# Kernel optimization log

Measured on AMD Instinct MI355X. Metric: run time of the kernel, lower is better.

The kernel has to match this reference:

```python
import math
import jax, jax.numpy as jnp
import numpy as np

T_LEN, BSZ, E_DIM, N_HEADS = 2048, 4, 768, 12


def setup_inputs() -> dict:
    key = jax.random.key(0)
    k0, k1, k2 = jax.random.split(key, 3)
    E = E_DIM
    return {
        "query": jax.random.normal(k0, (T_LEN, BSZ, E), dtype=jnp.float32),
        "attn_mask": jnp.zeros((T_LEN, T_LEN), dtype=jnp.float32),
        "in_proj_weight": jax.random.normal(k1, (3 * E, E), dtype=jnp.float32) * (1.0 / math.sqrt(E)),
        "in_proj_bias": jnp.zeros((3 * E,), dtype=jnp.float32),
        "out_proj_weight": jax.random.normal(k2, (E, E), dtype=jnp.float32) * (1.0 / math.sqrt(E)),
        "out_proj_bias": jnp.zeros((E,), dtype=jnp.float32),
        "num_heads": N_HEADS,
    }


def _rope_tables(seq_len, head_dim, dtype):
    # position_enc[pos, j] = pos / 10000**(2j/head_dim), j in [0, head_dim//2)
    pos = jnp.arange(seq_len, dtype=jnp.float32)[:, None]
    j = jnp.arange(head_dim // 2, dtype=jnp.float32)[None, :]
    ang = pos / jnp.power(jnp.float32(10000.0), 2.0 * j / head_dim)
    # stack([x, x], -1).reshape == repeat-interleave by 2 along last dim
    sin = jnp.repeat(jnp.sin(ang), 2, axis=-1).astype(dtype)  # (S, hd)
    cos = jnp.repeat(jnp.cos(ang), 2, axis=-1).astype(dtype)
    return sin, cos


def _rotate_half(x):
    # interleaved pairs: (x0, x1, x2, x3, ...) -> (-x1, x0, -x3, x2, ...)
    x_even = x[..., 0::2]
    x_odd = x[..., 1::2]
    return jnp.stack([-x_odd, x_even], axis=-1).reshape(x.shape)


def reference(query, attn_mask, in_proj_weight, in_proj_bias, out_proj_weight, out_proj_bias, num_heads):
    T, B, E = query.shape
    H = num_heads
    hd = E // H

    # fused QKV in-projection: (T, B, 3E)
    proj = jnp.einsum('tbe,fe->tbf', query, in_proj_weight) + in_proj_bias
    q, k, v = jnp.split(proj, 3, axis=-1)  # each (T, B, E)

    def to_bhtd(x):
        return jnp.transpose(x.reshape(T, B, H, hd), (1, 2, 0, 3))  # (B, H, T, hd)

    q, k, v = to_bhtd(q), to_bhtd(k), to_bhtd(v)

    sin, cos = _rope_tables(T, hd, q.dtype)  # (T, hd), broadcast over (B, H)
    q = q * cos + _rotate_half(q) * sin
    k = k * cos + _rotate_half(k) * sin

    scale = 1.0 / math.sqrt(hd)
    scores = jnp.einsum('bhtd,bhsd->bhts', q, k) * scale + attn_mask[None, None, :, :]
    attn = jax.nn.softmax(scores, axis=-1)
    out = jnp.einsum('bhts,bhsd->bhtd', attn, v)  # (B, H, T, hd)

    out = jnp.transpose(out, (2, 0, 1, 3)).reshape(T * B, E)  # (T*B, E)
    out = out @ out_proj_weight.T + out_proj_bias
    return out.reshape(T, B, E)
```

## Files before the change

kernel.cpp:

```cpp
#include <hip/hip_runtime.h>
#include <math.h>

#define TLEN 2048
#define BSZ  4
#define EDIM 768
#define NH   12
#define HD   64
#define NBH  (BSZ * NH)
#define LOG2E 1.44269504088896f

typedef __bf16 bf16;
typedef __bf16 bf16x8 __attribute__((ext_vector_type(8)));
typedef float  f32x4  __attribute__((ext_vector_type(4)));
typedef unsigned int uint;

__device__ __forceinline__ f32x4 mfma16(bf16x8 a, bf16x8 b, f32x4 c) {
  return __builtin_amdgcn_mfma_f32_16x16x32_bf16(a, b, c, 0, 0, 0);
}

__device__ __forceinline__ uint cvtpk(float lo, float hi) {
  uint r;
  asm("v_cvt_pk_bf16_f32 %0, %1, %2" : "=v"(r) : "v"(lo), "v"(hi));
  return r;
}

#define GLD16(gp, lp)                                                          \
  __builtin_amdgcn_global_load_lds(                                            \
      (const __attribute__((address_space(1))) uint32_t*)(gp),                 \
      (__attribute__((address_space(3))) uint32_t*)(lp), 16, 0, 0)

__device__ __forceinline__ bf16x8 ldsfrag(const bf16* t, int row, int kb) {
  return *reinterpret_cast<const bf16x8*>(
      (const char*)t + row * 128 + (kb ^ ((row & 7) << 4)));
}

#define CT_OFF   0x0u
#define ST_OFF   0x40000u
#define FLG_OFF  0x80000u
#define AQ_OFF   0x100000u
#define XB_OFF   0x100000u
#define QB_OFF   0xD00000u
#define KB_OFF   0x1900000u
#define VT_OFF   0x2500000u
#define WI_OFF   0x3100000u
#define WO_OFF   0x3460000u

#define QN8  786432
#define WIN8 221184
#define WON8 73728

__device__ __forceinline__ void cvt8(const float* __restrict__ s,
                                     bf16* __restrict__ d, int i) {
  const float4* sp = reinterpret_cast<const float4*>(s) + (size_t)i * 2;
  float4 a = sp[0], b = sp[1];
  bf16x8 o;
  o[0] = (bf16)a.x; o[1] = (bf16)a.y; o[2] = (bf16)a.z; o[3] = (bf16)a.w;
  o[4] = (bf16)b.x; o[5] = (bf16)b.y; o[6] = (bf16)b.z; o[7] = (bf16)b.w;
  reinterpret_cast<bf16x8*>(d)[i] = o;
}

__global__ __launch_bounds__(256) void prep_all_kernel(
    const float* __restrict__ q, bf16* __restrict__ qo,
    const float* __restrict__ wi, bf16* __restrict__ wio,
    const float* __restrict__ wo, bf16* __restrict__ woo,
    const float* __restrict__ mask, uint* __restrict__ flags,
    float* __restrict__ ct, float* __restrict__ st) {
  int bid = blockIdx.x;
  int tid = threadIdx.x;
  if (bid < 256) {
    int i = bid * 256 + tid;
    int t = i >> 5, j = i & 31;
    double ang = (double)t * pow(10000.0, -(double)j / 32.0);
    st[i] = (float)sin(ang);
    ct[i] = (float)cos(ang);
  } else if (bid < 4480) {
    int i = (bid - 256) * 256 + tid;
    if (i < QN8) { cvt8(q, qo, i); return; }
    int j = i - QN8;
    if (j < WIN8) { cvt8(wi, wio, j); return; }
    cvt8(wo, woo, j - WIN8);
  } else {
    int tile = bid - 4480;
    int ty = tile >> 5, tx = tile & 31;
    uint acc = 0;
#pragma unroll
    for (int i = 0; i < 4; ++i) {
      int c = tid + 256 * i;
      int rr = c >> 4, cc = (c & 15) * 4;
      float4 v = *reinterpret_cast<const float4*>(
          mask + (size_t)(ty * 64 + rr) * TLEN + tx * 64 + cc);
      acc |= __float_as_uint(v.x) | __float_as_uint(v.y) |
             __float_as_uint(v.z) | __float_as_uint(v.w);
    }
    unsigned long long b = __ballot(acc != 0);
    __shared__ uint red[4];
    if ((tid & 63) == 0) red[tid >> 6] = (b != 0ull) ? 1u : 0u;
    __syncthreads();
    if (tid == 0) flags[tile] = red[0] | red[1] | red[2] | red[3];
  }
}

template <int MODE>
__global__ __launch_bounds__(256) void gemm_bt(
    const bf16* __restrict__ A, const bf16* __restrict__ B,
    const float* __restrict__ bias,
    const float* __restrict__ ct, const float* __restrict__ st,
    bf16* __restrict__ qo, bf16* __restrict__ ko, bf16* __restrict__ vo,
    float* __restrict__ fo) {
  constexpr int K = EDIM;
  __shared__ __align__(16) bf16 As[128 * 64];
  __shared__ __align__(16) bf16 Bs[128 * 64];
  int tid = threadIdx.x;
  int lane = tid & 63, w = tid >> 6;
  int wr = w >> 1, wc = w & 1;
  int g = lane >> 4, cl = lane & 15;
  int bm = blockIdx.y, bn = blockIdx.x;
  int lrow = lane >> 3;
  int colb = ((lane & 7) ^ lrow) << 4;
  const char* Abase = (const char*)(A + (size_t)bm * 128 * K);
  const char* Bbase = (const char*)(B + (size_t)bn * 128 * K);

  f32x4 acc[4][4] = {};

  for (int kt = 0; kt < K; kt += 64) {
#pragma unroll
    for (int i = 0; i < 4; ++i) {
      int qi = w * 4 + i;
      int row = qi * 8 + lrow;
      GLD16(Abase + (size_t)row * (K * 2) + kt * 2 + colb, As + qi * 512 + lane * 8);
      GLD16(Bbase + (size_t)row * (K * 2) + kt * 2 + colb, Bs + qi * 512 + lane * 8);
    }
    __syncthreads();
#pragma unroll
    for (int kk = 0; kk < 2; ++kk) {
      bf16x8 af[4], bfr[4];
#pragma unroll
      for (int mi = 0; mi < 4; ++mi)
        af[mi] = ldsfrag(As, wr * 64 + mi * 16 + cl, kk * 64 + g * 16);
#pragma unroll
      for (int ni = 0; ni < 4; ++ni)
        bfr[ni] = ldsfrag(Bs, wc * 64 + ni * 16 + cl, kk * 64 + g * 16);
#pragma unroll
      for (int mi = 0; mi < 4; ++mi)
#pragma unroll
        for (int ni = 0; ni < 4; ++ni)
          acc[mi][ni] = mfma16(af[mi], bfr[ni], acc[mi][ni]);
    }
    __syncthreads();
  }

  if (MODE == 0) {
#pragma unroll
    for (int mi = 0; mi < 4; ++mi) {
      int mbase = bm * 128 + wr * 64 + mi * 16 + 4 * g;
      int t = mbase >> 2;
      int tl = t & 63;
      int tp = (t & ~63) + 32 * ((tl >> 5) & 1) + 8 * ((tl >> 2) & 3) +
               4 * ((tl >> 4) & 1) + (tl & 3);
#pragma unroll
      for (int ni = 0; ni < 4; ++ni) {
        int f = bn * 128 + wc * 64 + ni * 16 + cl;
        int sec = f / EDIM;
        int f0 = f - sec * EDIM;
        int h = f0 >> 6, d = f0 & 63;
        float bv = bias[f];
        float vals[4];
#pragma unroll
        for (int r = 0; r < 4; ++r) vals[r] = acc[mi][ni][r] + bv;
        if (sec < 2) {
          int j = d >> 1;
          float cv = ct[t * 32 + j], sv = st[t * 32 + j];
          bf16* dst = (sec == 0) ? qo : ko;
#pragma unroll
          for (int r = 0; r < 4; ++r) {
            float other = __shfl_xor(vals[r], 1);
            float rv = (d & 1) ? (vals[r] * cv + other * sv)
                               : (vals[r] * cv - other * sv);
            if (sec == 0) rv *= 0.125f * LOG2E;
            dst[(((size_t)r * NH + h) * TLEN + t) * HD + d] = (bf16)rv;
          }
        } else {
#pragma unroll
          for (int r = 0; r < 4; ++r)
            vo[(((size_t)r * NH + h) * HD + d) * TLEN + tp] = (bf16)vals[r];
        }
      }
    }
  } else {
#pragma unroll
    for (int mi = 0; mi < 4; ++mi) {
      int mbase = bm * 128 + wr * 64 + mi * 16 + 4 * g;
#pragma unroll
      for (int ni = 0; ni < 4; ++ni) {
        int n = bn * 128 + wc * 64 + ni * 16 + cl;
        float bv = bias[n];
#pragma unroll
        for (int r = 0; r < 4; ++r)
          fo[(size_t)(mbase + r) * EDIM + n] = acc[mi][ni][r] + bv;
      }
    }
  }
}

__global__ __launch_bounds__(512) void attn_kernel(
    const bf16* __restrict__ qa, const bf16* __restrict__ ka,
    const bf16* __restrict__ vt, const float* __restrict__ mask,
    const uint* __restrict__ flags, bf16* __restrict__ xo) {
  __shared__ __align__(16) bf16 Ks[2][4096];
  __shared__ __align__(16) bf16 Vs[2][4096];
  int tid = threadIdx.x;
  int lane = tid & 63, w = tid >> 6;
  int g = lane >> 4, cl = lane & 15;
  int lin = blockIdx.y * 16 + blockIdx.x;
  int lin2 = (lin & 7) * 96 + (lin >> 3);
  int qt = lin2 & 15, bh = lin2 >> 4;
  int qrow0 = qt * 128 + w * 16;
  const bf16* qbh = qa + (size_t)bh * TLEN * HD;
  const char* kbase = (const char*)(ka + (size_t)bh * TLEN * HD);
  const char* vbase = (const char*)(vt + (size_t)bh * HD * TLEN);
  int lrow = lane >> 3;
  int colb = ((lane & 7) ^ lrow) << 4;
  int sw = w & 3;
  const uint* flgrow = flags + (qrow0 >> 6) * 32;

  bf16x8 qf[2];
#pragma unroll
  for (int h = 0; h < 2; ++h)
    qf[h] = *reinterpret_cast<const bf16x8*>(
        qbh + (size_t)(qrow0 + cl) * HD + h * 32 + g * 8);

  bf16x8 ones;
#pragma unroll
  for (int j = 0; j < 8; ++j) ones[j] = (bf16)1.0f;

  f32x4 o[4] = {};
  f32x4 oden = {};
  float mrow = -1e30f;

#pragma unroll
  for (int i = 0; i < 2; ++i) {
    int qi = sw * 2 + i;
    int row = qi * 8 + lrow;
    if (w < 4)
      GLD16(kbase + (size_t)row * 128 + colb, &Ks[0][qi * 512 + lane * 8]);
    else
      GLD16(vbase + (size_t)row * (TLEN * 2) + colb, &Vs[0][qi * 512 + lane * 8]);
  }
  __syncthreads();

  for (int stile = 0; stile < TLEN / 64; ++stile) {
    int cur = stile & 1;
    if (stile + 1 < TLEN / 64) {
      int s1 = (stile + 1) * 64;
#pragma unroll
      for (int i = 0; i < 2; ++i) {
        int qi = sw * 2 + i;
        int row = qi * 8 + lrow;
        if (w < 4)
          GLD16(kbase + (size_t)(s1 + row) * 128 + colb,
                &Ks[cur ^ 1][qi * 512 + lane * 8]);
        else
          GLD16(vbase + (size_t)row * (TLEN * 2) + s1 * 2 + colb,
                &Vs[cur ^ 1][qi * 512 + lane * 8]);
      }
    }
    const bf16* Kc = Ks[cur];
    const bf16* Vc = Vs[cur];

    f32x4 sc[4];
#pragma unroll
    for (int ni = 0; ni < 4; ++ni) {
      bf16x8 k0 = ldsfrag(Kc, ni * 16 + cl, g * 16);
      bf16x8 k1 = ldsfrag(Kc, ni * 16 + cl, 64 + g * 16);
      f32x4 z = {};
      z = mfma16(k0, qf[0], z);
      z = mfma16(k1, qf[1], z);
      sc[ni] = z;
    }

    if (flgrow[stile]) {
      int q = qrow0 + cl;
#pragma unroll
      for (int ni = 0; ni < 4; ++ni)
#pragma unroll
        for (int r = 0; r < 4; ++r)
          sc[ni][r] = fmaf(mask[(size_t)q * TLEN + stile * 64 + ni * 16 + 4 * g + r],
                           LOG2E, sc[ni][r]);
    }

    float ml = fmaxf(fmaxf(fmaxf(sc[0][0], sc[0][1]), fmaxf(sc[0][2], sc[0][3])),
                     fmaxf(fmaxf(sc[1][0], sc[1][1]), fmaxf(sc[1][2], sc[1][3])));
    ml = fmaxf(ml,
               fmaxf(fmaxf(fmaxf(sc[2][0], sc[2][1]), fmaxf(sc[2][2], sc[2][3])),
                     fmaxf(fmaxf(sc[3][0], sc[3][1]), fmaxf(sc[3][2], sc[3][3]))));
    if (!__all(ml <= mrow + 11.54f)) {
      float mfull = fmaxf(ml, __shfl_xor(ml, 16));
      mfull = fmaxf(mfull, __shfl_xor(mfull, 32));
      float mn = fmaxf(mrow, mfull);
      float al = exp2f(mrow - mn);
      mrow = mn;
#pragma unroll
      for (int di = 0; di < 4; ++di)
#pragma unroll
        for (int r = 0; r < 4; ++r) o[di][r] *= al;
#pragma unroll
      for (int r = 0; r < 4; ++r) oden[r] *= al;
    }

    union { uint u[4]; bf16x8 v; } f0, f1;
#pragma unroll
    for (int ni = 0; ni < 4; ++ni) {
      float p0 = exp2f(sc[ni][0] - mrow);
      float p1 = exp2f(sc[ni][1] - mrow);
      float p2 = exp2f(sc[ni][2] - mrow);
      float p3 = exp2f(sc[ni][3] - mrow);
      uint lo = cvtpk(p0, p1);
      uint hi2 = cvtpk(p2, p3);
      if (ni < 2) { f0.u[2 * ni] = lo; f0.u[2 * ni + 1] = hi2; }
      else        { f1.u[2 * (ni - 2)] = lo; f1.u[2 * (ni - 2) + 1] = hi2; }
    }

#pragma unroll
    for (int di = 0; di < 4; ++di) {
      int row = di * 16 + cl;
      bf16x8 v0 = ldsfrag(Vc, row, g * 16);
      bf16x8 v1 = ldsfrag(Vc, row, 64 + g * 16);
      o[di] = mfma16(v0, f0.v, o[di]);
      o[di] = mfma16(v1, f1.v, o[di]);
    }
    oden = mfma16(ones, f0.v, oden);
    oden = mfma16(ones, f1.v, oden);

    __syncthreads();
  }

  int b = bh / NH, h = bh % NH;
  int t = qrow0 + cl;
  float inv = 1.0f / oden[0];
  bf16* dst = xo + (size_t)(t * BSZ + b) * EDIM + h * HD + 4 * g;
#pragma unroll
  for (int di = 0; di < 4; ++di) {
    union { bf16 hh[4]; uint2 u; } w4;
#pragma unroll
    for (int r = 0; r < 4; ++r) w4.hh[r] = (bf16)(o[di][r] * inv);
    *reinterpret_cast<uint2*>(dst + di * 16) = w4.u;
  }
}

extern "C" void kernel_launch(void* const* d_in, const int* in_sizes, int n_in,
                              void* d_out, int out_size, void* d_ws, size_t ws_size,
                              hipStream_t stream) {
  const float* query = (const float*)d_in[0];
  const float* mask  = (const float*)d_in[1];
  const float* win   = (const float*)d_in[2];
  const float* bin   = (const float*)d_in[3];
  const float* wout  = (const float*)d_in[4];
  const float* bout  = (const float*)d_in[5];
  (void)in_sizes; (void)n_in; (void)out_size; (void)ws_size;

  char* ws = (char*)d_ws;
  float* ct   = (float*)(ws + CT_OFF);
  float* st   = (float*)(ws + ST_OFF);
  uint*  flg  = (uint*)(ws + FLG_OFF);
  bf16*  aq   = (bf16*)(ws + AQ_OFF);
  bf16*  qb   = (bf16*)(ws + QB_OFF);
  bf16*  kb   = (bf16*)(ws + KB_OFF);
  bf16*  vtb  = (bf16*)(ws + VT_OFF);
  bf16*  xb   = (bf16*)(ws + XB_OFF);
  bf16*  wib  = (bf16*)(ws + WI_OFF);
  bf16*  wob  = (bf16*)(ws + WO_OFF);
  float* out  = (float*)d_out;

  prep_all_kernel<<<dim3(5504), dim3(256), 0, stream>>>(
      query, aq, win, wib, wout, wob, mask, flg, ct, st);

  gemm_bt<0><<<dim3(3 * EDIM / 128, TLEN * BSZ / 128), dim3(256), 0, stream>>>(
      aq, wib, bin, ct, st, qb, kb, vtb, nullptr);

  attn_kernel<<<dim3(TLEN / 128, NBH), dim3(512), 0, stream>>>(
      qb, kb, vtb, mask, flg, xb);

  gemm_bt<1><<<dim3(EDIM / 128, TLEN * BSZ / 128), dim3(256), 0, stream>>>(
      xb, wob, bout, nullptr, nullptr, nullptr, nullptr, nullptr, out);
}
```

Baseline: 283.0 us.

## Triple-buffer K/V tiles in attention with explicit vmcnt waits

Moves the attention kernel's K/V shared-memory staging from double to triple buffering. Loads are issued two tiles ahead, and the full __syncthreads is replaced by a partial s_waitcnt vmcnt plus a raw s_barrier, so one tile's loads can stay in flight across the barrier. It also rewrites the row-max reduction as a linear chain that can map onto fused 3-input max instructions. The cost is 50% more LDS per block, which may reduce occupancy, and the correctness of the vmcnt counts depends on each thread issuing exactly two loads per stage.

```diff
diff --git a/kernel.cpp b/kernel.cpp
--- a/kernel.cpp
+++ b/kernel.cpp
@@ -8,6 +8,7 @@
 #define HD   64
 #define NBH  (BSZ * NH)
 #define LOG2E 1.44269504088896f
+#define NT   (TLEN / 64)
 
 typedef __bf16 bf16;
 typedef __bf16 bf16x8 __attribute__((ext_vector_type(8)));
@@ -206,8 +207,8 @@
     const bf16* __restrict__ qa, const bf16* __restrict__ ka,
     const bf16* __restrict__ vt, const float* __restrict__ mask,
     const uint* __restrict__ flags, bf16* __restrict__ xo) {
-  __shared__ __align__(16) bf16 Ks[2][4096];
-  __shared__ __align__(16) bf16 Vs[2][4096];
+  __shared__ __align__(16) bf16 Ks[3][4096];
+  __shared__ __align__(16) bf16 Vs[3][4096];
   int tid = threadIdx.x;
   int lane = tid & 63, w = tid >> 6;
   int g = lane >> 4, cl = lane & 15;
@@ -223,6 +224,20 @@
   int sw = w & 3;
   const uint* flgrow = flags + (qrow0 >> 6) * 32;
 
+  auto stage = [&](int st, int buf) {
+#pragma unroll
+    for (int i = 0; i < 2; ++i) {
+      int qi = sw * 2 + i;
+      int row = qi * 8 + lrow;
+      if (w < 4)
+        GLD16(kbase + (size_t)(st * 64 + row) * 128 + colb,
+              &Ks[buf][qi * 512 + lane * 8]);
+      else
+        GLD16(vbase + (size_t)row * (TLEN * 2) + st * 128 + colb,
+              &Vs[buf][qi * 512 + lane * 8]);
+    }
+  };
+
   bf16x8 qf[2];
 #pragma unroll
   for (int h = 0; h < 2; ++h)
@@ -237,33 +252,16 @@
   f32x4 oden = {};
   float mrow = -1e30f;
 
-#pragma unroll
-  for (int i = 0; i < 2; ++i) {
-    int qi = sw * 2 + i;
-    int row = qi * 8 + lrow;
-    if (w < 4)
-      GLD16(kbase + (size_t)row * 128 + colb, &Ks[0][qi * 512 + lane * 8]);
-    else
-      GLD16(vbase + (size_t)row * (TLEN * 2) + colb, &Vs[0][qi * 512 + lane * 8]);
-  }
-  __syncthreads();
-
-  for (int stile = 0; stile < TLEN / 64; ++stile) {
-    int cur = stile & 1;
-    if (stile + 1 < TLEN / 64) {
-      int s1 = (stile + 1) * 64;
-#pragma unroll
-      for (int i = 0; i < 2; ++i) {
-        int qi = sw * 2 + i;
-        int row = qi * 8 + lrow;
-        if (w < 4)
-          GLD16(kbase + (size_t)(s1 + row) * 128 + colb,
-                &Ks[cur ^ 1][qi * 512 + lane * 8]);
-        else
-          GLD16(vbase + (size_t)row * (TLEN * 2) + s1 * 2 + colb,
-                &Vs[cur ^ 1][qi * 512 + lane * 8]);
-      }
-    }
+  stage(0, 0);
+  stage(1, 1);
+  asm volatile("s_waitcnt vmcnt(2)" ::: "memory");
+  __builtin_amdgcn_sched_barrier(0);
+  __builtin_amdgcn_s_barrier();
+  __builtin_amdgcn_sched_barrier(0);
+
+  for (int stile = 0; stile < NT; ++stile) {
+    int cur = stile % 3;
+    if (stile + 2 < NT) stage(stile + 2, (stile + 2) % 3);
     const bf16* Kc = Ks[cur];
     const bf16* Vc = Vs[cur];
 
@@ -288,11 +286,14 @@
                            LOG2E, sc[ni][r]);
     }
 
-    float ml = fmaxf(fmaxf(fmaxf(sc[0][0], sc[0][1]), fmaxf(sc[0][2], sc[0][3])),
-                     fmaxf(fmaxf(sc[1][0], sc[1][1]), fmaxf(sc[1][2], sc[1][3])));
-    ml = fmaxf(ml,
-               fmaxf(fmaxf(fmaxf(sc[2][0], sc[2][1]), fmaxf(sc[2][2], sc[2][3])),
-                     fmaxf(fmaxf(sc[3][0], sc[3][1]), fmaxf(sc[3][2], sc[3][3]))));
+    float ml = fmaxf(fmaxf(sc[0][0], sc[0][1]), sc[0][2]);
+    ml = fmaxf(fmaxf(ml, sc[0][3]), sc[1][0]);
+    ml = fmaxf(fmaxf(ml, sc[1][1]), sc[1][2]);
+    ml = fmaxf(fmaxf(ml, sc[1][3]), sc[2][0]);
+    ml = fmaxf(fmaxf(ml, sc[2][1]), sc[2][2]);
+    ml = fmaxf(fmaxf(ml, sc[2][3]), sc[3][0]);
+    ml = fmaxf(fmaxf(ml, sc[3][1]), sc[3][2]);
+    ml = fmaxf(ml, sc[3][3]);
     if (!__all(ml <= mrow + 11.54f)) {
       float mfull = fmaxf(ml, __shfl_xor(ml, 16));
       mfull = fmaxf(mfull, __shfl_xor(mfull, 32));
@@ -331,7 +332,14 @@
     oden = mfma16(ones, f0.v, oden);
     oden = mfma16(ones, f1.v, oden);
 
-    __syncthreads();
+    if (stile + 2 < NT) {
+      asm volatile("s_waitcnt vmcnt(2)" ::: "memory");
+    } else {
+      asm volatile("s_waitcnt vmcnt(0)" ::: "memory");
+    }
+    __builtin_amdgcn_sched_barrier(0);
+    __builtin_amdgcn_s_barrier();
+    __builtin_amdgcn_sched_barrier(0);
   }
 
   int b = bh / NH, h = bh % NH;
```

New measurement: 288.5 us. Within noise of the previous version (+1.9%).
